# Performance work log

Hardware: AMD Instinct MI355X
Metric: run time of the kernel (lower is better)

The kernel has to match this reference:

```python
import jax, jax.numpy as jnp
import numpy as np

D_ENC = 512
D_DEC = 512
D_JOINT = D_ENC + D_DEC  # 1024
V = 1024


def setup_inputs() -> dict:
    key = jax.random.key(0)
    ks = jax.random.split(key, 8)
    s = lambda fan_in: 1.0 / np.sqrt(fan_in)
    return {
        "encoder_output": jax.random.normal(ks[0], (8, 200, D_ENC), dtype=jnp.float32),
        "decoder_output": jax.random.normal(ks[1], (8, 50, D_DEC), dtype=jnp.float32),
        "W_enc": jax.random.uniform(ks[2], (D_JOINT, D_ENC), jnp.float32, -s(D_ENC), s(D_ENC)),
        "b_enc": jax.random.uniform(ks[3], (D_JOINT,), jnp.float32, -s(D_ENC), s(D_ENC)),
        "W_dec": jax.random.uniform(ks[4], (D_JOINT, D_DEC), jnp.float32, -s(D_DEC), s(D_DEC)),
        "b_dec": jax.random.uniform(ks[5], (D_JOINT,), jnp.float32, -s(D_DEC), s(D_DEC)),
        "W_fc": jax.random.uniform(ks[6], (V, D_JOINT), jnp.float32, -s(D_JOINT), s(D_JOINT)),
        "b_fc": jax.random.uniform(ks[7], (V,), jnp.float32, -s(D_JOINT), s(D_JOINT)),
    }


def reference(encoder_output, decoder_output, W_enc, b_enc, W_dec, b_dec, W_fc, b_fc):
    # enc: (B, T, D_JOINT); dec: (B, U, D_JOINT)
    enc = jnp.einsum('btd,jd->btj', encoder_output, W_enc) + b_enc
    dec = jnp.einsum('bud,jd->buj', decoder_output, W_dec) + b_dec
    # broadcast join: (B, T, U, D_JOINT)
    combined = enc[:, :, None, :] + dec[:, None, :, :]
    logits = jnp.einsum('btuj,vj->btuv', jnp.tanh(combined), W_fc) + b_fc
    return jax.nn.log_softmax(logits, axis=-1)
```

## Files before the change

kernel.cpp:

```cpp
#include <hip/hip_runtime.h>
#include <hip/hip_bf16.h>
#include <hip/hip_fp8.h>

#define TT 200
#define UU 50
#define BB 8
#define DJ 1024
#define DE 512
#define VV 1024
#define M_TOTAL (BB*TT*UU)
#define MB 80
#define NITER 32
#define WINV (1.0f/32.0f)

typedef float f32x4 __attribute__((ext_vector_type(4)));

__device__ __forceinline__ float fast_tanh(float x) {
    float e = __expf(2.f * x);
    return 1.f - 2.f / (e + 1.f);
}

__device__ __forceinline__ unsigned char f2fp8(float x) {
    return __hip_fp8_e4m3(x).__x;
}

__device__ __forceinline__ unsigned long long tanh_pack_fp8(float4 e0, float4 e1, float4 d0, float4 d1) {
    unsigned long long r;
    r  = (unsigned long long)f2fp8(fast_tanh(e0.x + d0.x));
    r |= (unsigned long long)f2fp8(fast_tanh(e0.y + d0.y)) << 8;
    r |= (unsigned long long)f2fp8(fast_tanh(e0.z + d0.z)) << 16;
    r |= (unsigned long long)f2fp8(fast_tanh(e0.w + d0.w)) << 24;
    r |= (unsigned long long)f2fp8(fast_tanh(e1.x + d1.x)) << 32;
    r |= (unsigned long long)f2fp8(fast_tanh(e1.y + d1.y)) << 40;
    r |= (unsigned long long)f2fp8(fast_tanh(e1.z + d1.z)) << 48;
    r |= (unsigned long long)f2fp8(fast_tanh(e1.w + d1.w)) << 56;
    return r;
}

__device__ __forceinline__ void gload_lds16(const unsigned char* g, unsigned char* l) {
    __builtin_amdgcn_global_load_lds(
        (const __attribute__((address_space(1))) unsigned int*)(const void*)g,
        (__attribute__((address_space(3))) unsigned int*)(void*)l, 16, 0, 0);
}

__global__ void k_wfct(const float* __restrict__ w, unsigned char* __restrict__ o) {
    const int G = blockIdx.x * 256 + threadIdx.x;
    const int gk = G >> 10, n = G & 1023;
    const float* src = w + (size_t)n * DJ + gk * 8;
    float4 a = *(const float4*)(src);
    float4 b = *(const float4*)(src + 4);
    unsigned long long r;
    r  = (unsigned long long)f2fp8(a.x * 32.f);
    r |= (unsigned long long)f2fp8(a.y * 32.f) << 8;
    r |= (unsigned long long)f2fp8(a.z * 32.f) << 16;
    r |= (unsigned long long)f2fp8(a.w * 32.f) << 24;
    r |= (unsigned long long)f2fp8(b.x * 32.f) << 32;
    r |= (unsigned long long)f2fp8(b.y * 32.f) << 40;
    r |= (unsigned long long)f2fp8(b.z * 32.f) << 48;
    r |= (unsigned long long)f2fp8(b.w * 32.f) << 56;
    *(unsigned long long*)(o + (size_t)G * 8) = r;
}

__global__ __launch_bounds__(256) void k_proj2(const float* __restrict__ enc,
                                               const float* __restrict__ dec,
                                               const float* __restrict__ W_enc,
                                               const float* __restrict__ b_enc,
                                               const float* __restrict__ W_dec,
                                               const float* __restrict__ b_dec,
                                               float* __restrict__ encp,
                                               float* __restrict__ decp) {
    __shared__ float in_s[16][DE];
    const bool isDec = blockIdx.x >= 100;
    const float* in  = isDec ? dec   : enc;
    const float* W   = isDec ? W_dec : W_enc;
    const float* bia = isDec ? b_dec : b_enc;
    float* out       = isDec ? decp  : encp;
    const int m0 = (isDec ? (blockIdx.x - 100) : blockIdx.x) * 16;
    const int tid = threadIdx.x;
    #pragma unroll
    for (int it = 0; it < 8; ++it) {
        int idx = tid + it * 256;
        int r = idx >> 7, c = (idx & 127) << 2;
        *(float4*)&in_s[r][c] = *(const float4*)(in + (size_t)(m0 + r) * DE + c);
    }
    __syncthreads();
    const int j = blockIdx.y * 256 + tid;
    const float4* wr = (const float4*)(W + (size_t)j * DE);
    float acc[16];
    #pragma unroll
    for (int r = 0; r < 16; ++r) acc[r] = 0.f;
    for (int d4 = 0; d4 < DE / 4; ++d4) {
        float4 w = wr[d4];
        #pragma unroll
        for (int r = 0; r < 16; ++r) {
            float4 x = *(const float4*)&in_s[r][d4 << 2];
            acc[r] += x.x * w.x + x.y * w.y + x.z * w.z + x.w * w.w;
        }
    }
    float bv = bia[j];
    #pragma unroll
    for (int r = 0; r < 16; ++r)
        out[(size_t)(m0 + r) * DJ + j] = acc[r] + bv;
}

__global__ __launch_bounds__(512, 2) void k_joint(const float* __restrict__ encp,
                                                  const float* __restrict__ decp,
                                                  const unsigned char* __restrict__ wfc8,
                                                  const float* __restrict__ bfc,
                                                  float* __restrict__ out) {
    __shared__ unsigned char Bs[3][32768];
    __shared__ unsigned char As[3][2560];
    __shared__ float red[8][MB];

    const int tid = threadIdx.x;
    const int wave = tid >> 6, lane = tid & 63;
    const int g = lane >> 4, ln = lane & 15;
    const int bid = blockIdx.x;
    const int m0 = bid * MB;

    const bool aRole = (tid < 320);
    const float *er = encp, *dr = decp;
    int agran = 0;
    if (aRole) {
        const int m = tid % MB;
        const int gk = tid / MB;
        const int mrow = m0 + m;
        const int b = mrow / (TT * UU);
        const int rem = mrow - b * (TT * UU);
        const int t = rem / UU;
        const int u = rem - t * UU;
        er = encp + (size_t)(b * TT + t) * DJ + gk * 8;
        dr = decp + (size_t)(b * UU + u) * DJ + gk * 8;
        agran = gk * MB + m;
    }

    f32x4 acc[5][8];
    #pragma unroll
    for (int mf = 0; mf < 5; ++mf)
        #pragma unroll
        for (int nf = 0; nf < 8; ++nf)
            acc[mf][nf] = (f32x4){0.f, 0.f, 0.f, 0.f};

    {
        const int kb0 = bid & 31, kb1 = (bid + 1) & 31;
        float4 e0, e1, d0, d1;
        if (aRole) {
            const int ko = kb0 << 5;
            e0 = *(const float4*)(er + ko);
            e1 = *(const float4*)(er + ko + 4);
            d0 = *(const float4*)(dr + ko);
            d1 = *(const float4*)(dr + ko + 4);
        }
        const unsigned char* s0 = wfc8 + (size_t)kb0 * 32768;
        #pragma unroll
        for (int r = 0; r < 4; ++r)
            gload_lds16(s0 + (r * 512 + tid) * 16, &Bs[0][(r * 512 + tid) * 16]);
        const unsigned char* s1 = wfc8 + (size_t)kb1 * 32768;
        #pragma unroll
        for (int r = 0; r < 4; ++r)
            gload_lds16(s1 + (r * 512 + tid) * 16, &Bs[1][(r * 512 + tid) * 16]);
        if (aRole)
            *(unsigned long long*)&As[0][(size_t)agran * 8] = tanh_pack_fp8(e0, e1, d0, d1);
    }

    for (int t = 0; t < NITER; ++t) {
        const int cb = t % 3;
        if (t < NITER - 1)
            asm volatile("s_waitcnt vmcnt(4) lgkmcnt(0)\n\ts_barrier" ::: "memory");
        else
            asm volatile("s_waitcnt vmcnt(0) lgkmcnt(0)\n\ts_barrier" ::: "memory");

        float4 e0, e1, d0, d1;
        const bool haveA = aRole && (t < NITER - 1);
        if (haveA) {
            const int ko = ((t + 1 + bid) & 31) << 5;
            e0 = *(const float4*)(er + ko);
            e1 = *(const float4*)(er + ko + 4);
            d0 = *(const float4*)(dr + ko);
            d1 = *(const float4*)(dr + ko + 4);
        }
        if (t < NITER - 2) {
            const unsigned char* src = wfc8 + (size_t)((t + 2 + bid) & 31) * 32768;
            #pragma unroll
            for (int r = 0; r < 4; ++r)
                gload_lds16(src + (r * 512 + tid) * 16, &Bs[(t + 2) % 3][(r * 512 + tid) * 16]);
        }

        __builtin_amdgcn_s_setprio(1);
        long afr[5];
        #pragma unroll
        for (int mf = 0; mf < 5; ++mf)
            afr[mf] = *(const long*)&As[cb][(size_t)(g * MB + mf * 16 + ln) * 8];
        #pragma unroll
        for (int nf = 0; nf < 8; ++nf) {
            long bfr = *(const long*)&Bs[cb][(size_t)(g * 1024 + wave * 128 + nf * 16 + ln) * 8];
            #pragma unroll
            for (int mf = 0; mf < 5; ++mf)
                acc[mf][nf] = __builtin_amdgcn_mfma_f32_16x16x32_fp8_fp8(afr[mf], bfr, acc[mf][nf], 0, 0, 0);
        }
        __builtin_amdgcn_s_setprio(0);

        if (haveA)
            *(unsigned long long*)&As[(t + 1) % 3][(size_t)agran * 8] = tanh_pack_fp8(e0, e1, d0, d1);
    }

    float bv[8];
    #pragma unroll
    for (int nf = 0; nf < 8; ++nf) bv[nf] = bfc[wave * 128 + nf * 16 + ln];
    #pragma unroll
    for (int mf = 0; mf < 5; ++mf)
        #pragma unroll
        for (int nf = 0; nf < 8; ++nf)
            #pragma unroll
            for (int j = 0; j < 4; ++j)
                acc[mf][nf][j] = acc[mf][nf][j] * WINV + bv[nf];

    float rmx[5][4];
    #pragma unroll
    for (int mf = 0; mf < 5; ++mf)
        #pragma unroll
        for (int j = 0; j < 4; ++j) {
            float mx = -3.0e38f;
            #pragma unroll
            for (int nf = 0; nf < 8; ++nf) mx = fmaxf(mx, acc[mf][nf][j]);
            #pragma unroll
            for (int s = 1; s < 16; s <<= 1) mx = fmaxf(mx, __shfl_xor(mx, s));
            rmx[mf][j] = mx;
        }
    if (ln == 0) {
        #pragma unroll
        for (int mf = 0; mf < 5; ++mf)
            #pragma unroll
            for (int j = 0; j < 4; ++j)
                red[wave][mf * 16 + g * 4 + j] = rmx[mf][j];
    }
    __syncthreads();
    #pragma unroll
    for (int mf = 0; mf < 5; ++mf)
        #pragma unroll
        for (int j = 0; j < 4; ++j) {
            const int r = mf * 16 + g * 4 + j;
            float mx = red[0][r];
            #pragma unroll
            for (int w = 1; w < 8; ++w) mx = fmaxf(mx, red[w][r]);
            rmx[mf][j] = mx;
        }
    __syncthreads();

    float rsm[5][4];
    #pragma unroll
    for (int mf = 0; mf < 5; ++mf)
        #pragma unroll
        for (int j = 0; j < 4; ++j) {
            float s = 0.f;
            #pragma unroll
            for (int nf = 0; nf < 8; ++nf) s += __expf(acc[mf][nf][j] - rmx[mf][j]);
            #pragma unroll
            for (int t2 = 1; t2 < 16; t2 <<= 1) s += __shfl_xor(s, t2);
            rsm[mf][j] = s;
        }
    if (ln == 0) {
        #pragma unroll
        for (int mf = 0; mf < 5; ++mf)
            #pragma unroll
            for (int j = 0; j < 4; ++j)
                red[wave][mf * 16 + g * 4 + j] = rsm[mf][j];
    }
    __syncthreads();
    #pragma unroll
    for (int mf = 0; mf < 5; ++mf)
        #pragma unroll
        for (int j = 0; j < 4; ++j) {
            const int r = mf * 16 + g * 4 + j;
            float s = 0.f;
            #pragma unroll
            for (int w = 0; w < 8; ++w) s += red[w][r];
            const float lse = rmx[mf][j] + __logf(s);
            float* op = out + (size_t)(m0 + r) * VV + wave * 128 + ln;
            #pragma unroll
            for (int nf = 0; nf < 8; ++nf)
                __builtin_nontemporal_store(acc[mf][nf][j] - lse, op + nf * 16);
        }
}

extern "C" void kernel_launch(void* const* d_in, const int* in_sizes, int n_in,
                              void* d_out, int out_size, void* d_ws, size_t ws_size,
                              hipStream_t stream) {
    const float* enc   = (const float*)d_in[0];
    const float* dec   = (const float*)d_in[1];
    const float* W_enc = (const float*)d_in[2];
    const float* b_enc = (const float*)d_in[3];
    const float* W_dec = (const float*)d_in[4];
    const float* b_dec = (const float*)d_in[5];
    const float* W_fc  = (const float*)d_in[6];
    const float* b_fc  = (const float*)d_in[7];
    float* out = (float*)d_out;

    float* encp = (float*)d_ws;
    float* decp = encp + (size_t)BB * TT * DJ;
    unsigned char* wfc8 = (unsigned char*)(decp + (size_t)BB * UU * DJ);

    k_wfct<<<(VV * DJ) / (256 * 8), 256, 0, stream>>>(W_fc, wfc8);
    k_proj2<<<dim3(125, DJ / 256), 256, 0, stream>>>(enc, dec, W_enc, b_enc, W_dec, b_dec, encp, decp);
    k_joint<<<M_TOTAL / MB, 512, 0, stream>>>(encp, decp, wfc8, b_fc, out);
}
```

Measured before the change: 402.0 us.

## Precompute full fp8 A tile up front and double-buffer B with phased loads

The projection kernel now writes enc/dec outputs in a k-granule-major layout (8-float groups), so the joint kernel can load contiguous chunks. The joint kernel converts the whole 80x1024 tanh(enc+dec) fp8 A tile into LDS once before the main loop, instead of streaming it per k-step with dedicated threads. The B tiles now use double buffering, with the next tile's loads split into four phases interleaved with MFMA groups and separated by barriers. This removes the per-iteration A conversion work and the triple-buffer bookkeeping, but uses more LDS (80KB A plus 64KB B), which may reduce occupancy, and adds more barriers per iteration.

```diff
diff --git a/kernel.cpp b/kernel.cpp
--- a/kernel.cpp
+++ b/kernel.cpp
@@ -75,6 +75,7 @@
     const float* W   = isDec ? W_dec : W_enc;
     const float* bia = isDec ? b_dec : b_enc;
     float* out       = isDec ? decp  : encp;
+    const int NR     = isDec ? (BB*UU) : (BB*TT);
     const int m0 = (isDec ? (blockIdx.x - 100) : blockIdx.x) * 16;
     const int tid = threadIdx.x;
     #pragma unroll
@@ -98,9 +99,10 @@
         }
     }
     float bv = bia[j];
+    const int gk = j >> 3, kl = j & 7;
     #pragma unroll
     for (int r = 0; r < 16; ++r)
-        out[(size_t)(m0 + r) * DJ + j] = acc[r] + bv;
+        out[((size_t)gk * NR + (m0 + r)) * 8 + kl] = acc[r] + bv;
 }
 
 __global__ __launch_bounds__(512, 2) void k_joint(const float* __restrict__ encp,
@@ -108,8 +110,8 @@
                                                   const unsigned char* __restrict__ wfc8,
                                                   const float* __restrict__ bfc,
                                                   float* __restrict__ out) {
-    __shared__ unsigned char Bs[3][32768];
-    __shared__ unsigned char As[3][2560];
+    __shared__ unsigned char As[81920];
+    __shared__ unsigned char Bs[2][32768];
     __shared__ float red[8][MB];
 
     const int tid = threadIdx.x;
@@ -118,20 +120,28 @@
     const int bid = blockIdx.x;
     const int m0 = bid * MB;
 
-    const bool aRole = (tid < 320);
-    const float *er = encp, *dr = decp;
-    int agran = 0;
-    if (aRole) {
-        const int m = tid % MB;
-        const int gk = tid / MB;
+    {
+        const unsigned char* s0 = wfc8 + (size_t)(bid & 31) * 32768;
+        #pragma unroll
+        for (int r = 0; r < 4; ++r)
+            gload_lds16(s0 + (r * 512 + tid) * 16, &Bs[0][(r * 512 + tid) * 16]);
+    }
+    for (int r = 0; r < 20; ++r) {
+        const int gidx = r * 512 + tid;
+        const int gkf = gidx / MB;
+        const int m = gidx - gkf * MB;
         const int mrow = m0 + m;
         const int b = mrow / (TT * UU);
         const int rem = mrow - b * (TT * UU);
         const int t = rem / UU;
         const int u = rem - t * UU;
-        er = encp + (size_t)(b * TT + t) * DJ + gk * 8;
-        dr = decp + (size_t)(b * UU + u) * DJ + gk * 8;
-        agran = gk * MB + m;
+        const float* ep = encp + ((size_t)gkf * (BB * TT) + b * TT + t) * 8;
+        const float* dp = decp + ((size_t)gkf * (BB * UU) + b * UU + u) * 8;
+        float4 e0 = *(const float4*)(ep);
+        float4 e1 = *(const float4*)(ep + 4);
+        float4 d0 = *(const float4*)(dp);
+        float4 d1 = *(const float4*)(dp + 4);
+        *(unsigned long long*)&As[(size_t)gidx * 8] = tanh_pack_fp8(e0, e1, d0, d1);
     }
 
     f32x4 acc[5][8];
@@ -141,67 +151,48 @@
         for (int nf = 0; nf < 8; ++nf)
             acc[mf][nf] = (f32x4){0.f, 0.f, 0.f, 0.f};
 
-    {
-        const int kb0 = bid & 31, kb1 = (bid + 1) & 31;
-        float4 e0, e1, d0, d1;
-        if (aRole) {
-            const int ko = kb0 << 5;
-            e0 = *(const float4*)(er + ko);
-            e1 = *(const float4*)(er + ko + 4);
-            d0 = *(const float4*)(dr + ko);
-            d1 = *(const float4*)(dr + ko + 4);
-        }
-        const unsigned char* s0 = wfc8 + (size_t)kb0 * 32768;
-        #pragma unroll
-        for (int r = 0; r < 4; ++r)
-            gload_lds16(s0 + (r * 512 + tid) * 16, &Bs[0][(r * 512 + tid) * 16]);
-        const unsigned char* s1 = wfc8 + (size_t)kb1 * 32768;
-        #pragma unroll
-        for (int r = 0; r < 4; ++r)
-            gload_lds16(s1 + (r * 512 + tid) * 16, &Bs[1][(r * 512 + tid) * 16]);
-        if (aRole)
-            *(unsigned long long*)&As[0][(size_t)agran * 8] = tanh_pack_fp8(e0, e1, d0, d1);
-    }
-
     for (int t = 0; t < NITER; ++t) {
-        const int cb = t % 3;
-        if (t < NITER - 1)
-            asm volatile("s_waitcnt vmcnt(4) lgkmcnt(0)\n\ts_barrier" ::: "memory");
-        else
-            asm volatile("s_waitcnt vmcnt(0) lgkmcnt(0)\n\ts_barrier" ::: "memory");
-
-        float4 e0, e1, d0, d1;
-        const bool haveA = aRole && (t < NITER - 1);
-        if (haveA) {
-            const int ko = ((t + 1 + bid) & 31) << 5;
-            e0 = *(const float4*)(er + ko);
-            e1 = *(const float4*)(er + ko + 4);
-            d0 = *(const float4*)(dr + ko);
-            d1 = *(const float4*)(dr + ko + 4);
-        }
-        if (t < NITER - 2) {
-            const unsigned char* src = wfc8 + (size_t)((t + 2 + bid) & 31) * 32768;
-            #pragma unroll
-            for (int r = 0; r < 4; ++r)
-                gload_lds16(src + (r * 512 + tid) * 16, &Bs[(t + 2) % 3][(r * 512 + tid) * 16]);
-        }
-
-        __builtin_amdgcn_s_setprio(1);
+        const int cur = t & 1, nxt = cur ^ 1;
+        const int kb = (t + bid) & 31;
+        const unsigned char* srcN = wfc8 + (size_t)((t + 1 + bid) & 31) * 32768;
+        if (t < NITER - 1) {
+            gload_lds16(srcN + (size_t)tid * 16, &Bs[nxt][(size_t)tid * 16]);
+            asm volatile("s_waitcnt vmcnt(1) lgkmcnt(0)" ::: "memory");
+        } else {
+            asm volatile("s_waitcnt vmcnt(0) lgkmcnt(0)" ::: "memory");
+        }
+        __builtin_amdgcn_sched_barrier(0);
+        __builtin_amdgcn_s_barrier();
+
         long afr[5];
         #pragma unroll
-        for (int mf = 0; mf < 5; ++mf)
-            afr[mf] = *(const long*)&As[cb][(size_t)(g * MB + mf * 16 + ln) * 8];
-        #pragma unroll
-        for (int nf = 0; nf < 8; ++nf) {
-            long bfr = *(const long*)&Bs[cb][(size_t)(g * 1024 + wave * 128 + nf * 16 + ln) * 8];
-            #pragma unroll
-            for (int mf = 0; mf < 5; ++mf)
-                acc[mf][nf] = __builtin_amdgcn_mfma_f32_16x16x32_fp8_fp8(afr[mf], bfr, acc[mf][nf], 0, 0, 0);
-        }
-        __builtin_amdgcn_s_setprio(0);
-
-        if (haveA)
-            *(unsigned long long*)&As[(t + 1) % 3][(size_t)agran * 8] = tanh_pack_fp8(e0, e1, d0, d1);
+        for (int ph = 0; ph < 4; ++ph) {
+            if (ph == 0) {
+                #pragma unroll
+                for (int mf = 0; mf < 5; ++mf)
+                    afr[mf] = *(const long*)&As[(size_t)((kb * 4 + g) * MB + mf * 16 + ln) * 8];
+            }
+            long bfr[2];
+            #pragma unroll
+            for (int q = 0; q < 2; ++q)
+                bfr[q] = *(const long*)&Bs[cur][(size_t)(g * 1024 + wave * 128 + (ph * 2 + q) * 16 + ln) * 8];
+            if (t < NITER - 1 && ph < 3)
+                gload_lds16(srcN + (size_t)((ph + 1) * 512 + tid) * 16,
+                            &Bs[nxt][(size_t)((ph + 1) * 512 + tid) * 16]);
+            __builtin_amdgcn_sched_barrier(0);
+            __builtin_amdgcn_s_barrier();
+            asm volatile("s_waitcnt lgkmcnt(0)" ::: "memory");
+            __builtin_amdgcn_sched_barrier(0);
+            __builtin_amdgcn_s_setprio(1);
+            #pragma unroll
+            for (int q = 0; q < 2; ++q)
+                #pragma unroll
+                for (int mf = 0; mf < 5; ++mf)
+                    acc[mf][ph * 2 + q] = __builtin_amdgcn_mfma_f32_16x16x32_fp8_fp8(afr[mf], bfr[q], acc[mf][ph * 2 + q], 0, 0, 0);
+            __builtin_amdgcn_s_setprio(0);
+            __builtin_amdgcn_sched_barrier(0);
+            __builtin_amdgcn_s_barrier();
+        }
     }
 
     float bv[8];
```

Result: faster. 373.8 us (-7.0%).
